# Performance work log

Hardware: AMD Instinct MI355X
Metric: run time of the kernel (lower is better)

## Reference

```python
import jax, jax.numpy as jnp
import numpy as np
from jax import lax

N_GROUPS = 2
TOPK_GROUPS = 1
TOPK = 4
ROUTE_SCALE = 1.0


def setup_inputs() -> dict:
    key = jax.random.key(0)
    k1, k2 = jax.random.split(key)
    T, D, E = 524288, 256, 64
    x = jax.random.normal(k1, (T, D), dtype=jnp.float32)
    W = jax.random.normal(k2, (E, D), dtype=jnp.float32) * 0.02  # router weight [out, in]
    return {"x": x, "W": W}


def reference(x, W):
    T = x.shape[0]
    E = W.shape[0]
    logits = x @ W.T  # [T, E]
    scores = jax.nn.softmax(logits.astype(jnp.float32), axis=-1)
    original_scores = scores
    # grouped masking (bias is None -> amax group score)
    g = scores.reshape(T, N_GROUPS, E // N_GROUPS)
    group_scores = g.max(axis=-1)  # [T, G]
    _, gidx = lax.top_k(group_scores, TOPK_GROUPS)  # [T, topk_groups]
    keep = jnp.zeros((T, N_GROUPS), dtype=bool).at[jnp.arange(T)[:, None], gidx].set(True)
    masked = jnp.where(keep[:, :, None], g, -jnp.inf).reshape(T, E)
    _, indices = lax.top_k(masked, TOPK)  # [T, topk]
    weights = jnp.take_along_axis(original_scores, indices, axis=1)
    weights = weights * ROUTE_SCALE
    return weights.astype(x.dtype), indices
```

## Files before the change

### kernel.cpp

```cpp
#include <hip/hip_runtime.h>
#include <hip/hip_bf16.h>
#include <stdint.h>


typedef __attribute__((ext_vector_type(8))) short bf16x8;
typedef __attribute__((ext_vector_type(4))) float f32x4;
typedef __attribute__((ext_vector_type(4))) int i32x4;

#define SPLIT_OFF 1024
#define LIST_OFF 102400
#define DELTA 1e-4f

__device__ __forceinline__ f32x4 mf(const i32x4& a, const i32x4& b,
                                    const f32x4& c) {
  return __builtin_amdgcn_mfma_f32_16x16x32_bf16(
      __builtin_bit_cast(bf16x8, a), __builtin_bit_cast(bf16x8, b), c, 0, 0, 0);
}

__device__ __forceinline__ int packhi(unsigned e0, unsigned e1) {
  return (int)__builtin_amdgcn_perm(e1, e0, 0x07060302u);
}

__device__ __forceinline__ void gload16(const void* g, void* l) {
  __builtin_amdgcn_global_load_lds(
      (const __attribute__((address_space(1))) void*)g,
      (__attribute__((address_space(3))) void*)l, 16, 0, 0);
}

__global__ void zero_meta(int* meta) { meta[0] = 0; }

__global__ void split_w(const float* __restrict__ W,
                        unsigned short* __restrict__ ws, int n) {
  int i = blockIdx.x * 256 + threadIdx.x;
  if (i >= n) return;
  float w = W[i];
  unsigned u = __float_as_uint(w);
  unsigned uh = u & 0xFFFF0000u;
  float rf = w - __uint_as_float(uh);
  unsigned short lv[2];
  lv[0] = (unsigned short)(uh >> 16);
  lv[1] = (unsigned short)(__float_as_uint(rf) >> 16);
  int e = i >> 8, k = i & 255;
  int nt = e >> 4, le = e & 15;
  int c = k >> 5, lg = (k >> 3) & 3, kk = k & 7;
  int lane = lg * 16 + le;
#pragma unroll
  for (int v = 0; v < 2; ++v)
    ws[(((c * 8 + v * 4 + nt) * 64) + lane) * 8 + kk] = lv[v];
}

struct XF2 { i32x4 h, m; };

__device__ __forceinline__ XF2 split2(f32x4 a, f32x4 b) {
  float xs[8] = {a[0], a[1], a[2], a[3], b[0], b[1], b[2], b[3]};
  XF2 f;
#pragma unroll
  for (int wd = 0; wd < 4; ++wd) {
    unsigned u0 = __float_as_uint(xs[2 * wd]);
    unsigned u1 = __float_as_uint(xs[2 * wd + 1]);
    f.h[wd] = packhi(u0, u1);
    float r0 = xs[2 * wd] - __uint_as_float(u0 & 0xFFFF0000u);
    float r1 = xs[2 * wd + 1] - __uint_as_float(u1 & 0xFFFF0000u);
    f.m[wd] = packhi(__float_as_uint(r0), __float_as_uint(r1));
  }
  return f;
}

#define GL(dst, ptr, OFFSTR)                                    \
  asm volatile("global_load_dwordx4 %0, %1, off offset:" OFFSTR \
               : "=v"(dst)                                      \
               : "v"(ptr))

#define WAITV(NSTR)                                         \
  do {                                                      \
    asm volatile("s_waitcnt vmcnt(" NSTR ")" ::: "memory"); \
    __builtin_amdgcn_sched_barrier(0);                      \
  } while (0)

__global__ __launch_bounds__(256, 2) void gate_kernel(
    const float* __restrict__ x, const unsigned short* __restrict__ wsp,
    float* __restrict__ out, int* __restrict__ meta, int* __restrict__ list,
    int cap, int T) {
  __shared__ i32x4 WL[4096];

  const int t = threadIdx.x;
  const int lane = t & 63;
  const int wid = t >> 6;
  const int le = lane & 15;
  const int lg = lane >> 4;
  const int tokbase = blockIdx.x * 256 + wid * 64;

  {
    const char* wsrc = (const char*)wsp + t * 16;
    char* wdst = (char*)WL + t * 16;
#pragma unroll
    for (int i = 0; i < 16; ++i) gload16(wsrc + i * 4096, wdst + i * 4096);
  }
  WAITV("0");
  __syncthreads();

  const float* xa[4];
#pragma unroll
  for (int t4 = 0; t4 < 4; ++t4)
    xa[t4] = x + (size_t)(tokbase + t4 * 16 + le) * 256 + lg * 8;

  f32x4 xbuf[3][8];
  f32x4 acc[4][4];
#pragma unroll
  for (int nt = 0; nt < 4; ++nt)
#pragma unroll
    for (int t4 = 0; t4 < 4; ++t4) acc[nt][t4] = (f32x4)0.0f;

#define STAGE_X(c)                                   \
  do {                                               \
    _Pragma("unroll") for (int t4 = 0; t4 < 4; ++t4) { \
      const float* p_ = xa[t4] + (c) * 32;           \
      GL(xbuf[(c) % 3][2 * t4], p_, "0");            \
      GL(xbuf[(c) % 3][2 * t4 + 1], p_, "16");       \
    }                                                \
  } while (0)

#define ITER(c, NSTR)                                             \
  {                                                               \
    if ((c) < 6) STAGE_X((c) + 2);                                \
    i32x4 wr[8];                                                  \
    _Pragma("unroll") for (int q = 0; q < 8; ++q)                 \
        wr[q] = WL[(((c) * 8 + q) << 6) + lane];                  \
    WAITV(NSTR);                                                  \
    _Pragma("unroll") for (int t4 = 0; t4 < 4; ++t4) {            \
      XF2 b = split2(xbuf[(c) % 3][2 * t4], xbuf[(c) % 3][2 * t4 + 1]); \
      _Pragma("unroll") for (int nt = 0; nt < 4; ++nt) {          \
        acc[nt][t4] = mf(wr[nt], b.h, acc[nt][t4]);               \
        acc[nt][t4] = mf(wr[nt], b.m, acc[nt][t4]);               \
        acc[nt][t4] = mf(wr[4 + nt], b.h, acc[nt][t4]);           \
        acc[nt][t4] = mf(wr[4 + nt], b.m, acc[nt][t4]);           \
      }                                                           \
    }                                                             \
  }

  STAGE_X(0);
  STAGE_X(1);
  ITER(0, "16");
  ITER(1, "16");
  ITER(2, "16");
  ITER(3, "16");
  ITER(4, "16");
  ITER(5, "16");
  ITER(6, "8");
  ITER(7, "0");

#pragma unroll
  for (int tt = 0; tt < 4; ++tt) {
    float l[16];
#pragma unroll
    for (int nt = 0; nt < 4; ++nt)
#pragma unroll
      for (int j = 0; j < 4; ++j) l[nt * 4 + j] = acc[nt][tt][j];

    float g0 = l[0], g1 = l[8];
#pragma unroll
    for (int j = 1; j < 8; ++j) {
      g0 = fmaxf(g0, l[j]);
      g1 = fmaxf(g1, l[8 + j]);
    }
    g0 = fmaxf(g0, __shfl_xor(g0, 16));
    g0 = fmaxf(g0, __shfl_xor(g0, 32));
    g1 = fmaxf(g1, __shfl_xor(g1, 16));
    g1 = fmaxf(g1, __shfl_xor(g1, 32));
    const int g = (g1 > g0) ? 1 : 0;
    const float m = fmaxf(g0, g1);

    float sum = 0.f;
#pragma unroll
    for (int k = 0; k < 16; ++k) sum += __expf(l[k] - m);
    sum += __shfl_xor(sum, 16);
    sum += __shfl_xor(sum, 32);
    const float inv = 1.0f / sum;

    float c[8];
    int ce[8];
#pragma unroll
    for (int j2 = 0; j2 < 8; ++j2) {
      c[j2] = l[g * 8 + j2];
      ce[j2] = (2 * g + (j2 >> 2)) * 16 + 4 * lg + (j2 & 3);
    }

    float v5[5];
    int e5[5];
#pragma unroll
    for (int it = 0; it < 5; ++it) {
      float bv = c[0];
      int be = ce[0];
#pragma unroll
      for (int j2 = 1; j2 < 8; ++j2) {
        bool gt = c[j2] > bv;
        bv = gt ? c[j2] : bv;
        be = gt ? ce[j2] : be;
      }
#pragma unroll
      for (int st = 0; st < 2; ++st) {
        int msk = 16 << st;
        float ov = __shfl_xor(bv, msk);
        int oe = __shfl_xor(be, msk);
        bool tk = (ov > bv) || (ov == bv && oe < be);
        bv = tk ? ov : bv;
        be = tk ? oe : be;
      }
      v5[it] = bv;
      e5[it] = be;
#pragma unroll
      for (int j2 = 0; j2 < 8; ++j2)
        c[j2] = (ce[j2] == be) ? -3.0e38f : c[j2];
    }

    float ming = fabsf(g0 - g1);
#pragma unroll
    for (int it = 0; it < 4; ++it) ming = fminf(ming, v5[it] - v5[it + 1]);

    if (lg == 0) {
      size_t trow = (size_t)tokbase + tt * 16 + le;
      *(float4*)&out[trow * 4] =
          make_float4(__expf(v5[0] - m) * inv, __expf(v5[1] - m) * inv,
                      __expf(v5[2] - m) * inv, __expf(v5[3] - m) * inv);
      *(float4*)&out[(size_t)T * 4 + trow * 4] = make_float4(
          (float)e5[0], (float)e5[1], (float)e5[2], (float)e5[3]);
      if (ming < DELTA) {
        int p = atomicAdd(meta, 1);
        if (p < cap) list[p] = (int)trow;
      }
    }
  }
}

__global__ __launch_bounds__(64) void fix_kernel(
    const float* __restrict__ x, const float* __restrict__ W,
    float* __restrict__ out, const int* __restrict__ meta,
    const int* __restrict__ list, int cap, int T) {
  const int e = threadIdx.x;
  int cnt = meta[0];
  cnt = cnt < cap ? cnt : cap;
  for (int i = blockIdx.x; i < cnt; i += gridDim.x) {
    const int tok = list[i];
    const float* xr = x + (size_t)tok * 256;
    const float* wr = W + (size_t)e * 256;
    float acc = 0.f;
#pragma unroll 8
    for (int d = 0; d < 256; d += 4) {
      float4 xv = *(const float4*)(xr + d);
      float4 wv = *(const float4*)(wr + d);
      acc = fmaf(xv.x, wv.x, acc);
      acc = fmaf(xv.y, wv.y, acc);
      acc = fmaf(xv.z, wv.z, acc);
      acc = fmaf(xv.w, wv.w, acc);
    }
    float gm = acc;
#pragma unroll
    for (int st = 0; st < 5; ++st) gm = fmaxf(gm, __shfl_xor(gm, 1 << st));
    float om = __shfl_xor(gm, 32);
    float g0 = (e < 32) ? gm : om;
    float g1 = (e < 32) ? om : gm;
    const int g = (g1 > g0) ? 1 : 0;
    const float m = fmaxf(g0, g1);
    float sum = __expf(acc - m);
#pragma unroll
    for (int st = 0; st < 6; ++st) sum += __shfl_xor(sum, 1 << st);
    const float inv = 1.0f / sum;

    float cand = ((e >> 5) == g) ? acc : -3.0e38f;
    float w4[4], i4[4];
#pragma unroll
    for (int it = 0; it < 4; ++it) {
      float bv = cand;
      int be = e;
#pragma unroll
      for (int st = 0; st < 6; ++st) {
        int msk = 1 << st;
        float ov = __shfl_xor(bv, msk);
        int oe = __shfl_xor(be, msk);
        bool tk = (ov > bv) || (ov == bv && oe < be);
        bv = tk ? ov : bv;
        be = tk ? oe : be;
      }
      w4[it] = __expf(bv - m) * inv;
      i4[it] = (float)be;
      if (e == be) cand = -3.0e38f;
    }
    if (e == 0) {
      *(float4*)&out[(size_t)tok * 4] = make_float4(w4[0], w4[1], w4[2], w4[3]);
      *(float4*)&out[(size_t)T * 4 + (size_t)tok * 4] =
          make_float4(i4[0], i4[1], i4[2], i4[3]);
    }
  }
}

extern "C" void kernel_launch(void* const* d_in, const int* in_sizes, int n_in,
                              void* d_out, int out_size, void* d_ws,
                              size_t ws_size, hipStream_t stream) {
  const float* x = (const float*)d_in[0];
  const float* W = (const float*)d_in[1];
  float* out = (float*)d_out;
  int T = in_sizes[0] / 256;
  int nW = in_sizes[1];
  int* meta = (int*)d_ws;
  unsigned short* wsp = (unsigned short*)((char*)d_ws + SPLIT_OFF);
  int* list = (int*)((char*)d_ws + LIST_OFF);
  int cap = (ws_size > LIST_OFF + 4) ? (int)((ws_size - LIST_OFF) / 4) : 0;
  hipLaunchKernelGGL(zero_meta, dim3(1), dim3(1), 0, stream, meta);
  hipLaunchKernelGGL(split_w, dim3((nW + 255) / 256), dim3(256), 0, stream, W,
                     wsp, nW);
  hipLaunchKernelGGL(gate_kernel, dim3(T / 256), dim3(256), 0, stream, x, wsp,
                     out, meta, list, cap, T);
  hipLaunchKernelGGL(fix_kernel, dim3(2048), dim3(64), 0, stream, x, W, out,
                     meta, list, cap, T);
}
```

Baseline: 148.1 us.

## Deepen x prefetch to four stages and overlap with weight LDS load

```diff
diff --git a/kernel.cpp b/kernel.cpp
--- a/kernel.cpp
+++ b/kernel.cpp
@@ -66,10 +66,10 @@
   return f;
 }
 
-#define GL(dst, ptr, OFFSTR)                                    \
-  asm volatile("global_load_dwordx4 %0, %1, off offset:" OFFSTR \
-               : "=v"(dst)                                      \
-               : "v"(ptr))
+#define GL(dst, ptr, OFF)                                     \
+  asm volatile("global_load_dwordx4 %0, %1, off offset:%2"    \
+               : "=v"(dst)                                    \
+               : "v"(ptr), "n"(OFF))
 
 #define WAITV(NSTR)                                         \
   do {                                                      \
@@ -90,61 +90,65 @@
   const int lg = lane >> 4;
   const int tokbase = blockIdx.x * 256 + wid * 64;
 
+  const float* xa0 = x + (size_t)(tokbase + le) * 256 + lg * 8;
+  const float* xa1 = xa0 + 16 * 256;
+  const float* xa2 = xa0 + 32 * 256;
+  const float* xa3 = xa0 + 48 * 256;
+
+  f32x4 xbuf[4][8];
+  f32x4 acc[4][4];
+#pragma unroll
+  for (int nt = 0; nt < 4; ++nt)
+#pragma unroll
+    for (int t4 = 0; t4 < 4; ++t4) acc[nt][t4] = (f32x4)0.0f;
+
+#define STAGE_X(c)                              \
+  do {                                          \
+    GL(xbuf[(c) & 3][0], xa0, (c) * 128);       \
+    GL(xbuf[(c) & 3][1], xa0, (c) * 128 + 16);  \
+    GL(xbuf[(c) & 3][2], xa1, (c) * 128);       \
+    GL(xbuf[(c) & 3][3], xa1, (c) * 128 + 16);  \
+    GL(xbuf[(c) & 3][4], xa2, (c) * 128);       \
+    GL(xbuf[(c) & 3][5], xa2, (c) * 128 + 16);  \
+    GL(xbuf[(c) & 3][6], xa3, (c) * 128);       \
+    GL(xbuf[(c) & 3][7], xa3, (c) * 128 + 16);  \
+  } while (0)
+
+#define ITER(c, NSTR)                                                   \
+  {                                                                     \
+    if ((c) + 3 < 8) STAGE_X((c) + 3);                                  \
+    i32x4 wr[8];                                                        \
+    _Pragma("unroll") for (int q = 0; q < 8; ++q)                       \
+        wr[q] = WL[(((c) * 8 + q) << 6) + lane];                        \
+    WAITV(NSTR);                                                        \
+    _Pragma("unroll") for (int t4 = 0; t4 < 4; ++t4) {                  \
+      XF2 b = split2(xbuf[(c) & 3][2 * t4], xbuf[(c) & 3][2 * t4 + 1]); \
+      _Pragma("unroll") for (int nt = 0; nt < 4; ++nt) {                \
+        acc[nt][t4] = mf(wr[nt], b.h, acc[nt][t4]);                     \
+        acc[nt][t4] = mf(wr[nt], b.m, acc[nt][t4]);                     \
+        acc[nt][t4] = mf(wr[4 + nt], b.h, acc[nt][t4]);                 \
+        acc[nt][t4] = mf(wr[4 + nt], b.m, acc[nt][t4]);                 \
+      }                                                                 \
+    }                                                                   \
+  }
+
   {
     const char* wsrc = (const char*)wsp + t * 16;
     char* wdst = (char*)WL + t * 16;
 #pragma unroll
     for (int i = 0; i < 16; ++i) gload16(wsrc + i * 4096, wdst + i * 4096);
   }
-  WAITV("0");
-  __syncthreads();
-
-  const float* xa[4];
-#pragma unroll
-  for (int t4 = 0; t4 < 4; ++t4)
-    xa[t4] = x + (size_t)(tokbase + t4 * 16 + le) * 256 + lg * 8;
-
-  f32x4 xbuf[3][8];
-  f32x4 acc[4][4];
-#pragma unroll
-  for (int nt = 0; nt < 4; ++nt)
-#pragma unroll
-    for (int t4 = 0; t4 < 4; ++t4) acc[nt][t4] = (f32x4)0.0f;
-
-#define STAGE_X(c)                                   \
-  do {                                               \
-    _Pragma("unroll") for (int t4 = 0; t4 < 4; ++t4) { \
-      const float* p_ = xa[t4] + (c) * 32;           \
-      GL(xbuf[(c) % 3][2 * t4], p_, "0");            \
-      GL(xbuf[(c) % 3][2 * t4 + 1], p_, "16");       \
-    }                                                \
-  } while (0)
-
-#define ITER(c, NSTR)                                             \
-  {                                                               \
-    if ((c) < 6) STAGE_X((c) + 2);                                \
-    i32x4 wr[8];                                                  \
-    _Pragma("unroll") for (int q = 0; q < 8; ++q)                 \
-        wr[q] = WL[(((c) * 8 + q) << 6) + lane];                  \
-    WAITV(NSTR);                                                  \
-    _Pragma("unroll") for (int t4 = 0; t4 < 4; ++t4) {            \
-      XF2 b = split2(xbuf[(c) % 3][2 * t4], xbuf[(c) % 3][2 * t4 + 1]); \
-      _Pragma("unroll") for (int nt = 0; nt < 4; ++nt) {          \
-        acc[nt][t4] = mf(wr[nt], b.h, acc[nt][t4]);               \
-        acc[nt][t4] = mf(wr[nt], b.m, acc[nt][t4]);               \
-        acc[nt][t4] = mf(wr[4 + nt], b.h, acc[nt][t4]);           \
-        acc[nt][t4] = mf(wr[4 + nt], b.m, acc[nt][t4]);           \
-      }                                                           \
-    }                                                             \
-  }
-
   STAGE_X(0);
   STAGE_X(1);
-  ITER(0, "16");
-  ITER(1, "16");
-  ITER(2, "16");
-  ITER(3, "16");
-  ITER(4, "16");
+  STAGE_X(2);
+  WAITV("24");
+  __builtin_amdgcn_s_barrier();
+
+  ITER(0, "24");
+  ITER(1, "24");
+  ITER(2, "24");
+  ITER(3, "24");
+  ITER(4, "24");
   ITER(5, "16");
   ITER(6, "8");
   ITER(7, "0");
```

Result: no change. 145.7 us (-1.6%).
